# Optimization experiments

Hardware: AMD Instinct MI355X
Metric: run time of the kernel (lower is better)

## Reference

```python
import jax, jax.numpy as jnp
import numpy as np
import math

HAD = 1024  # hadamard_size hard-coded in HiggsLinear

def _hadamard_matrix(n):
    H = np.array([[1.0]], dtype=np.float32)
    while H.shape[0] < n:
        H = np.block([[H, H], [H, -H]])
    return H

# normalized Hadamard (scale = 1/sqrt(1024)); symmetric, so x @ _H == H x per block
_H = jnp.asarray(_hadamard_matrix(HAD) / math.sqrt(HAD))

def setup_inputs() -> dict:
    key = jax.random.key(0)
    k1, k2, k3, k4, k5 = jax.random.split(key, 5)
    in_f, out_f, d, n_codes, tokens = 4096, 4096, 2, 256, 8192
    return {
        "x": jax.random.normal(k1, (tokens, in_f), jnp.float32),
        "codes": jax.random.randint(k2, (out_f, in_f // d), 0, n_codes, jnp.int32),
        "grid": jax.random.normal(k3, (n_codes, d), jnp.float32),
        "scales": jax.random.uniform(k4, (out_f, in_f // HAD), jnp.float32, 0.5, 1.5),
        "bias": jax.random.normal(k5, (out_f,), jnp.float32),
    }

def reference(x, codes, grid, scales, bias):
    d = grid.shape[1]
    out_f = codes.shape[0]
    post = ((HAD - 1) // d + 1) * d  # post_hadamard_size
    # --- dequantize weight: codebook gather + per-hadamard-group scale ---
    W = grid[codes]                               # (out, num_higgs_groups, d)
    W = W.reshape(out_f, -1, post)[..., :HAD]     # (out, n_had_groups, 1024)
    W = W * scales[..., None]
    W = W.reshape(out_f, -1)                      # (out, in)
    # --- blockwise Hadamard transform of input (block = 1024) ---
    nh = x.shape[-1] // HAD
    xh = x.reshape(x.shape[:-1] + (nh, HAD)) @ _H
    xh = xh.reshape(x.shape[:-1] + (nh * HAD,))
    # --- fused dequant matmul equivalent: F.linear(xh, W, bias) ---
    return xh @ W.T + bias
```

## Files before the change

### kernel.cpp

```cpp
#include <hip/hip_runtime.h>

#define M_TOK 8192
#define N_OUT 4096
#define K_IN  4096

typedef __bf16 bf16x8 __attribute__((ext_vector_type(8)));
typedef float f32x4 __attribute__((ext_vector_type(4)));

__device__ __forceinline__ unsigned short f2b(float f) {
  union { float f; unsigned u; } c; c.f = f;
  unsigned u = c.u;
  return (unsigned short)((u + 0x7FFFu + ((u >> 16) & 1u)) >> 16);
}

__global__ __launch_bounds__(256) void cvt_x_kernel(const float* __restrict__ x,
                                                    unsigned short* __restrict__ xb) {
  long i = ((long)blockIdx.x * 256 + threadIdx.x) * 8;
  float4 a = *(const float4*)(x + i);
  float4 b = *(const float4*)(x + i + 4);
  union { unsigned short us[8]; uint4 v; } o;
  o.us[0] = f2b(a.x); o.us[1] = f2b(a.y); o.us[2] = f2b(a.z); o.us[3] = f2b(a.w);
  o.us[4] = f2b(b.x); o.us[5] = f2b(b.y); o.us[6] = f2b(b.z); o.us[7] = f2b(b.w);
  *(uint4*)(xb + i) = o.v;
}

__global__ __launch_bounds__(256) void dequant_had_kernel(const int* __restrict__ codes,
                                                          const float* __restrict__ grid,
                                                          const float* __restrict__ scales,
                                                          unsigned short* __restrict__ Wt) {
  int o = blockIdx.x >> 2;
  int g = blockIdx.x & 3;
  int t = threadIdx.x;
  __shared__ float buf[1024];
  const int* crow = codes + (long)o * 2048 + g * 512;
  int2 cc = ((const int2*)crow)[t];
  float2 g0 = ((const float2*)grid)[cc.x];
  float2 g1 = ((const float2*)grid)[cc.y];
  buf[4 * t + 0] = g0.x; buf[4 * t + 1] = g0.y;
  buf[4 * t + 2] = g1.x; buf[4 * t + 3] = g1.y;
#pragma unroll
  for (int s = 0; s < 10; s++) {
    __syncthreads();
#pragma unroll
    for (int r = 0; r < 2; r++) {
      int p = t + (r << 8);
      int i = ((p >> s) << (s + 1)) | (p & ((1 << s) - 1));
      int j = i | (1 << s);
      float a = buf[i], b = buf[j];
      buf[i] = a + b;
      buf[j] = a - b;
    }
  }
  __syncthreads();
  float sc = scales[o * 4 + g] * 0.03125f;
  unsigned short* wrow = Wt + (long)o * 4096 + g * 1024;
#pragma unroll
  for (int r = 0; r < 4; r++) {
    int e = t + (r << 8);
    wrow[e] = f2b(buf[e] * sc);
  }
}

__device__ __forceinline__ void load16_to_lds(const unsigned short* g, unsigned short* l) {
  __builtin_amdgcn_global_load_lds((const __attribute__((address_space(1))) void*)g,
                                   (__attribute__((address_space(3))) void*)l,
                                   16, 0, 0);
}

__global__ __launch_bounds__(256, 2) void gemm_kernel(const unsigned short* __restrict__ A,
                                                      const unsigned short* __restrict__ B,
                                                      const float* __restrict__ bias,
                                                      float* __restrict__ C) {
  __shared__ unsigned short sA[128 * 32];
  __shared__ unsigned short sB[128 * 32];
  const int bm = blockIdx.y * 128;
  const int bn = blockIdx.x * 128;
  const int tid = threadIdx.x;
  const int wave = tid >> 6;
  const int lane = tid & 63;
  const int wm = (wave >> 1) * 64;
  const int wn = (wave & 1) * 64;

  const int srow = lane >> 2;
  const int scol = (lane & 3) * 8;
  const long K = K_IN;
  const unsigned short* Ag0 = A + (long)(bm + wave * 16 + srow) * K + scol;
  const unsigned short* Ag1 = A + (long)(bm + (wave + 4) * 16 + srow) * K + scol;
  const unsigned short* Bg0 = B + (long)(bn + wave * 16 + srow) * K + scol;
  const unsigned short* Bg1 = B + (long)(bn + (wave + 4) * 16 + srow) * K + scol;
  unsigned short* lA0 = &sA[(wave * 16) * 32];
  unsigned short* lA1 = &sA[((wave + 4) * 16) * 32];
  unsigned short* lB0 = &sB[(wave * 16) * 32];
  unsigned short* lB1 = &sB[((wave + 4) * 16) * 32];

  f32x4 acc[4][4] = {};

  const int frow = lane & 15;
  const int fk = (lane >> 4) * 8;

  for (int k0 = 0; k0 < K_IN; k0 += 32) {
    __syncthreads();
    load16_to_lds(Ag0 + k0, lA0);
    load16_to_lds(Ag1 + k0, lA1);
    load16_to_lds(Bg0 + k0, lB0);
    load16_to_lds(Bg1 + k0, lB1);
    __syncthreads();
    bf16x8 af[4], bfr[4];
#pragma unroll
    for (int i = 0; i < 4; i++)
      af[i] = *(const bf16x8*)&sA[(wm + i * 16 + frow) * 32 + fk];
#pragma unroll
    for (int i = 0; i < 4; i++)
      bfr[i] = *(const bf16x8*)&sB[(wn + i * 16 + frow) * 32 + fk];
#pragma unroll
    for (int mi = 0; mi < 4; mi++)
#pragma unroll
      for (int ni = 0; ni < 4; ni++)
        acc[mi][ni] = __builtin_amdgcn_mfma_f32_16x16x32_bf16(af[mi], bfr[ni], acc[mi][ni], 0, 0, 0);
  }

  const int cn = lane & 15;
  const int cm = (lane >> 4) * 4;
#pragma unroll
  for (int ni = 0; ni < 4; ni++) {
    const int col = bn + wn + ni * 16 + cn;
    const float bb = bias[col];
#pragma unroll
    for (int mi = 0; mi < 4; mi++) {
#pragma unroll
      for (int r = 0; r < 4; r++) {
        const int row = bm + wm + mi * 16 + cm + r;
        C[(long)row * N_OUT + col] = acc[mi][ni][r] + bb;
      }
    }
  }
}

extern "C" void kernel_launch(void* const* d_in, const int* in_sizes, int n_in,
                              void* d_out, int out_size, void* d_ws, size_t ws_size,
                              hipStream_t stream) {
  const float* x      = (const float*)d_in[0];
  const int*   codes  = (const int*)d_in[1];
  const float* grid   = (const float*)d_in[2];
  const float* scales = (const float*)d_in[3];
  const float* bias   = (const float*)d_in[4];
  float* out = (float*)d_out;

  unsigned short* xb = (unsigned short*)d_ws;
  unsigned short* Wt = xb + (size_t)M_TOK * K_IN;

  cvt_x_kernel<<<(M_TOK * (long)K_IN) / (256 * 8), 256, 0, stream>>>(x, xb);
  dequant_had_kernel<<<N_OUT * 4, 256, 0, stream>>>(codes, grid, scales, Wt);
  gemm_kernel<<<dim3(N_OUT / 128, M_TOK / 128), 256, 0, stream>>>(xb, Wt, bias, out);
}
```

Before: 574.7 us.

## Merge prep kernels, do Hadamard in registers/shuffles, swizzle GEMM LDS layout

Merges the x-to-bf16 conversion and the weight dequant+Hadamard into one launch. The Hadamard now runs per wave: each lane holds 16 values, does the in-register butterflies, then cross-lane shuffle stages, which removes the shared-memory passes and block barriers. The GEMM's direct-to-LDS loads are remapped to an XOR-swizzled chunk layout so the fragment reads hit fewer LDS bank conflicts. This costs some added index arithmetic and a wave-wide shuffle dependency.

```diff
diff --git a/kernel.cpp b/kernel.cpp
--- a/kernel.cpp
+++ b/kernel.cpp
@@ -3,6 +3,8 @@
 #define M_TOK 8192
 #define N_OUT 4096
 #define K_IN  4096
+#define CVT_BLOCKS ((M_TOK * K_IN) / 2048)
+#define DEQ_BLOCKS (N_OUT * 4 / 4)
 
 typedef __bf16 bf16x8 __attribute__((ext_vector_type(8)));
 typedef float f32x4 __attribute__((ext_vector_type(4)));
@@ -13,51 +15,68 @@
   return (unsigned short)((u + 0x7FFFu + ((u >> 16) & 1u)) >> 16);
 }
 
-__global__ __launch_bounds__(256) void cvt_x_kernel(const float* __restrict__ x,
-                                                    unsigned short* __restrict__ xb) {
-  long i = ((long)blockIdx.x * 256 + threadIdx.x) * 8;
-  float4 a = *(const float4*)(x + i);
-  float4 b = *(const float4*)(x + i + 4);
-  union { unsigned short us[8]; uint4 v; } o;
-  o.us[0] = f2b(a.x); o.us[1] = f2b(a.y); o.us[2] = f2b(a.z); o.us[3] = f2b(a.w);
-  o.us[4] = f2b(b.x); o.us[5] = f2b(b.y); o.us[6] = f2b(b.z); o.us[7] = f2b(b.w);
-  *(uint4*)(xb + i) = o.v;
-}
-
-__global__ __launch_bounds__(256) void dequant_had_kernel(const int* __restrict__ codes,
-                                                          const float* __restrict__ grid,
-                                                          const float* __restrict__ scales,
-                                                          unsigned short* __restrict__ Wt) {
-  int o = blockIdx.x >> 2;
-  int g = blockIdx.x & 3;
-  int t = threadIdx.x;
-  __shared__ float buf[1024];
-  const int* crow = codes + (long)o * 2048 + g * 512;
-  int2 cc = ((const int2*)crow)[t];
-  float2 g0 = ((const float2*)grid)[cc.x];
-  float2 g1 = ((const float2*)grid)[cc.y];
-  buf[4 * t + 0] = g0.x; buf[4 * t + 1] = g0.y;
-  buf[4 * t + 2] = g1.x; buf[4 * t + 3] = g1.y;
+__global__ __launch_bounds__(256) void prep_kernel(const float* __restrict__ x,
+                                                   unsigned short* __restrict__ xb,
+                                                   const int* __restrict__ codes,
+                                                   const float* __restrict__ grid,
+                                                   const float* __restrict__ scales,
+                                                   unsigned short* __restrict__ Wt) {
+  if (blockIdx.x < CVT_BLOCKS) {
+    long i = ((long)blockIdx.x * 256 + threadIdx.x) * 8;
+    float4 a = *(const float4*)(x + i);
+    float4 b = *(const float4*)(x + i + 4);
+    union { unsigned short us[8]; uint4 v; } o;
+    o.us[0] = f2b(a.x); o.us[1] = f2b(a.y); o.us[2] = f2b(a.z); o.us[3] = f2b(a.w);
+    o.us[4] = f2b(b.x); o.us[5] = f2b(b.y); o.us[6] = f2b(b.z); o.us[7] = f2b(b.w);
+    *(uint4*)(xb + i) = o.v;
+  } else {
+    int bid = blockIdx.x - CVT_BLOCKS;
+    int wave = threadIdx.x >> 6;
+    int lane = threadIdx.x & 63;
+    int G = bid * 4 + wave;
+    int o = G >> 2;
+    int g = G & 3;
+    const int* crow = codes + (long)o * 2048 + g * 512 + lane * 8;
+    int4 c0 = *(const int4*)crow;
+    int4 c1 = *(const int4*)(crow + 4);
+    float v[16];
+    const float2* g2p = (const float2*)grid;
+    float2 t;
+    t = g2p[c0.x]; v[0] = t.x;  v[1] = t.y;
+    t = g2p[c0.y]; v[2] = t.x;  v[3] = t.y;
+    t = g2p[c0.z]; v[4] = t.x;  v[5] = t.y;
+    t = g2p[c0.w]; v[6] = t.x;  v[7] = t.y;
+    t = g2p[c1.x]; v[8] = t.x;  v[9] = t.y;
+    t = g2p[c1.y]; v[10] = t.x; v[11] = t.y;
+    t = g2p[c1.z]; v[12] = t.x; v[13] = t.y;
+    t = g2p[c1.w]; v[14] = t.x; v[15] = t.y;
 #pragma unroll
-  for (int s = 0; s < 10; s++) {
-    __syncthreads();
+    for (int s = 1; s < 16; s <<= 1) {
 #pragma unroll
-    for (int r = 0; r < 2; r++) {
-      int p = t + (r << 8);
-      int i = ((p >> s) << (s + 1)) | (p & ((1 << s) - 1));
-      int j = i | (1 << s);
-      float a = buf[i], b = buf[j];
-      buf[i] = a + b;
-      buf[j] = a - b;
+      for (int base = 0; base < 16; base++) {
+        if (!(base & s)) {
+          float a = v[base], b = v[base | s];
+          v[base] = a + b;
+          v[base | s] = a - b;
+        }
+      }
     }
-  }
-  __syncthreads();
-  float sc = scales[o * 4 + g] * 0.03125f;
-  unsigned short* wrow = Wt + (long)o * 4096 + g * 1024;
 #pragma unroll
-  for (int r = 0; r < 4; r++) {
-    int e = t + (r << 8);
-    wrow[e] = f2b(buf[e] * sc);
+    for (int m = 1; m <= 32; m <<= 1) {
+      bool hi = (lane & m) != 0;
+#pragma unroll
+      for (int c = 0; c < 16; c++) {
+        float p = __shfl_xor(v[c], m, 64);
+        v[c] = hi ? p - v[c] : p + v[c];
+      }
+    }
+    float sc = scales[o * 4 + g] * 0.03125f;
+    union { unsigned short us[16]; uint4 q[2]; } out;
+#pragma unroll
+    for (int c = 0; c < 16; c++) out.us[c] = f2b(v[c] * sc);
+    unsigned short* wp = Wt + (long)o * 4096 + g * 1024 + lane * 16;
+    *(uint4*)wp = out.q[0];
+    *(uint4*)(wp + 8) = out.q[1];
   }
 }
 
@@ -81,8 +100,8 @@
   const int wm = (wave >> 1) * 64;
   const int wn = (wave & 1) * 64;
 
-  const int srow = lane >> 2;
-  const int scol = (lane & 3) * 8;
+  const int srow = lane & 15;
+  const int scol = ((lane >> 4) ^ (lane & 3)) * 8;
   const long K = K_IN;
   const unsigned short* Ag0 = A + (long)(bm + wave * 16 + srow) * K + scol;
   const unsigned short* Ag1 = A + (long)(bm + (wave + 4) * 16 + srow) * K + scol;
@@ -95,8 +114,9 @@
 
   f32x4 acc[4][4] = {};
 
-  const int frow = lane & 15;
-  const int fk = (lane >> 4) * 8;
+  const int achunk = (wave >> 1) * 4;
+  const int bchunk = (wave & 1) * 4;
+  const int fslot = ((((lane >> 4) ^ (lane & 3)) * 16) + (lane & 15)) * 8;
 
   for (int k0 = 0; k0 < K_IN; k0 += 32) {
     __syncthreads();
@@ -108,10 +128,10 @@
     bf16x8 af[4], bfr[4];
 #pragma unroll
     for (int i = 0; i < 4; i++)
-      af[i] = *(const bf16x8*)&sA[(wm + i * 16 + frow) * 32 + fk];
+      af[i] = *(const bf16x8*)&sA[(achunk + i) * 512 + fslot];
 #pragma unroll
     for (int i = 0; i < 4; i++)
-      bfr[i] = *(const bf16x8*)&sB[(wn + i * 16 + frow) * 32 + fk];
+      bfr[i] = *(const bf16x8*)&sB[(bchunk + i) * 512 + fslot];
 #pragma unroll
     for (int mi = 0; mi < 4; mi++)
 #pragma unroll
@@ -149,7 +169,6 @@
   unsigned short* xb = (unsigned short*)d_ws;
   unsigned short* Wt = xb + (size_t)M_TOK * K_IN;
 
-  cvt_x_kernel<<<(M_TOK * (long)K_IN) / (256 * 8), 256, 0, stream>>>(x, xb);
-  dequant_had_kernel<<<N_OUT * 4, 256, 0, stream>>>(codes, grid, scales, Wt);
+  prep_kernel<<<CVT_BLOCKS + DEQ_BLOCKS, 256, 0, stream>>>(x, xb, codes, grid, scales, Wt);
   gemm_kernel<<<dim3(N_OUT / 128, M_TOK / 128), 256, 0, stream>>>(xb, Wt, bias, out);
 }
```

Result: faster. 557.5 us (-3.0%).
